# Kernel tuning notes

Measured on AMD Instinct MI355X. Metric: run time of the kernel, lower is better.

## Reference

```python
import jax, jax.numpy as jnp
import numpy as np
from jax import lax

T, B = 256, 64
VOCAB, EMB, HID, NLAB = 100000, 300, 256, 20
PAD_WORD = 0


def setup_inputs() -> dict:
    key = jax.random.key(0)
    ks = jax.random.split(key, 16)
    sentences = jax.random.randint(ks[0], (T, B), 0, VOCAB)
    sentences = sentences.at[0].set(jnp.maximum(sentences[0], 1))  # mask[0] must be all on (torchcrf)
    labels = jax.random.randint(ks[1], (T, B), 0, NLAB)
    s = 0.05
    emb = jax.random.normal(ks[2], (VOCAB, EMB), jnp.float32) * s
    Wih_f = jax.random.normal(ks[3], (4 * HID, EMB), jnp.float32) * s
    Whh_f = jax.random.normal(ks[4], (4 * HID, HID), jnp.float32) * s
    b_f = jax.random.normal(ks[5], (4 * HID,), jnp.float32) * s
    Wih_b = jax.random.normal(ks[6], (4 * HID, EMB), jnp.float32) * s
    Whh_b = jax.random.normal(ks[7], (4 * HID, HID), jnp.float32) * s
    b_b = jax.random.normal(ks[8], (4 * HID,), jnp.float32) * s
    W_top = jax.random.normal(ks[9], (NLAB, 2 * HID), jnp.float32) * s
    b_top = jax.random.normal(ks[10], (NLAB,), jnp.float32) * s
    start_t = jax.random.normal(ks[11], (NLAB,), jnp.float32) * 0.1
    end_t = jax.random.normal(ks[12], (NLAB,), jnp.float32) * 0.1
    trans = jax.random.normal(ks[13], (NLAB, NLAB), jnp.float32) * 0.1
    return dict(emb=emb, Wih_f=Wih_f, Whh_f=Whh_f, b_f=b_f, Wih_b=Wih_b,
                Whh_b=Whh_b, b_b=b_b, W_top=W_top, b_top=b_top,
                start_t=start_t, end_t=end_t, trans=trans,
                sentences=sentences, labels=labels)


def _lstm_dir(x, W_ih, W_hh, b, reverse):
    # x: (T, B, E) -> hs: (T, B, H); torch gate order i,f,g,o
    H = W_hh.shape[1]
    x_proj = jnp.einsum('tbe,ge->tbg', x, W_ih) + b  # precompute input projection

    def step(carry, xp):
        h, c = carry
        gates = xp + h @ W_hh.T
        i, f, g, o = jnp.split(gates, 4, axis=-1)
        c = jax.nn.sigmoid(f) * c + jax.nn.sigmoid(i) * jnp.tanh(g)
        h = jax.nn.sigmoid(o) * jnp.tanh(c)
        return (h, c), h

    init = (jnp.zeros((x.shape[1], H), x.dtype), jnp.zeros((x.shape[1], H), x.dtype))
    _, hs = lax.scan(step, init, x_proj, reverse=reverse)
    return hs


def _crf_nll(emissions, tags, mask, start_t, end_t, trans):
    # emissions: (T,B,L), tags: (T,B), mask: (T,B) bool. torchcrf math, reduction='sum'.
    Tn, Bn, L = emissions.shape
    maskf = mask.astype(emissions.dtype)
    barange = jnp.arange(Bn)
    # numerator
    score = start_t[tags[0]] + emissions[0, barange, tags[0]]
    trans_sc = trans[tags[:-1], tags[1:]]  # (T-1, B)
    emit_sc = jnp.take_along_axis(emissions[1:], tags[1:, :, None], axis=2)[..., 0]
    score = score + ((trans_sc + emit_sc) * maskf[1:]).sum(0)
    seq_ends = mask.astype(jnp.int32).sum(0) - 1  # (B,)
    last_tags = jnp.take_along_axis(tags, seq_ends[None, :], axis=0)[0]
    score = score + end_t[last_tags]
    # partition (log-sum-exp forward recurrence)
    alpha0 = start_t[None, :] + emissions[0]  # (B, L)

    def step(alpha, inp):
        emis_t, m_t = inp
        nxt = jax.nn.logsumexp(alpha[:, :, None] + trans[None] + emis_t[:, None, :], axis=1)
        return jnp.where(m_t[:, None], nxt, alpha), None

    alpha, _ = lax.scan(step, alpha0, (emissions[1:], mask[1:]))
    denom = jax.nn.logsumexp(alpha + end_t[None, :], axis=1)
    llh = (score - denom).sum()
    return -llh


def reference(emb, Wih_f, Whh_f, b_f, Wih_b, Whh_b, b_b, W_top, b_top,
              start_t, end_t, trans, sentences, labels):
    x = emb[sentences]  # (T, B, E)
    h_f = _lstm_dir(x, Wih_f, Whh_f, b_f, reverse=False)
    h_b = _lstm_dir(x, Wih_b, Whh_b, b_b, reverse=True)
    rnn_out = jnp.concatenate([h_f, h_b], axis=-1)  # (T, B, 2H)
    emissions = jnp.einsum('tbh,lh->tbl', rnn_out, W_top) + b_top
    mask = sentences != PAD_WORD
    return _crf_nll(emissions, labels, mask, start_t, end_t, trans)
```

## Files before the change

### kernel.cpp

```cpp
#include <hip/hip_runtime.h>
#include <hip/hip_bf16.h>

#define T_    256
#define B_    64
#define EMB_  300
#define HID_  256
#define G_    1024
#define L_    20
#define M_    (T_*B_)

#define NCL   32
#define CLB   8
#define BPC   4
#define UPB   32

typedef float f32x4 __attribute__((ext_vector_type(4)));
typedef unsigned long long u64;

__global__ __launch_bounds__(256) void k_xproj(
    const float* __restrict__ emb,
    const float* __restrict__ Wih_f, const float* __restrict__ b_f,
    const float* __restrict__ Wih_b, const float* __restrict__ b_b,
    const int*   __restrict__ sent,
    float* __restrict__ xp)
{
    __shared__ float As[16][68];
    __shared__ float Bs[16][68];
    __shared__ int   words[64];

    const int tid = threadIdx.x;
    const int n0  = blockIdx.x * 64;
    const int m0  = blockIdx.y * 64;
    const int dir = n0 >> 10;
    const int g0  = n0 & 1023;
    const float* __restrict__ Wih  = dir ? Wih_b : Wih_f;
    const float* __restrict__ bias = dir ? b_b   : b_f;

    if (tid < 64) words[tid] = sent[m0 + tid];
    __syncthreads();

    const int r = tid >> 2;
    const int q = tid & 3;
    const float* aptr = emb + (size_t)words[r] * EMB_ + q * 4;
    const float* bptr = Wih + (size_t)(g0 + r) * EMB_ + q * 4;

    const int tx = tid & 15;
    const int ty = tid >> 4;
    float acc[4][4] = {};

    for (int k0 = 0; k0 < 304; k0 += 16) {
        const int k = k0 + q * 4;
        float4 av = make_float4(0.f, 0.f, 0.f, 0.f);
        float4 bv = make_float4(0.f, 0.f, 0.f, 0.f);
        if (k < 300) {
            av = *(const float4*)(aptr + k0);
            bv = *(const float4*)(bptr + k0);
        }
        As[q*4+0][r] = av.x; As[q*4+1][r] = av.y; As[q*4+2][r] = av.z; As[q*4+3][r] = av.w;
        Bs[q*4+0][r] = bv.x; Bs[q*4+1][r] = bv.y; Bs[q*4+2][r] = bv.z; Bs[q*4+3][r] = bv.w;
        __syncthreads();
        #pragma unroll
        for (int kk = 0; kk < 16; ++kk) {
            const float4 a = *(const float4*)&As[kk][ty * 4];
            const float4 b = *(const float4*)&Bs[kk][tx * 4];
            acc[0][0] += a.x*b.x; acc[0][1] += a.x*b.y; acc[0][2] += a.x*b.z; acc[0][3] += a.x*b.w;
            acc[1][0] += a.y*b.x; acc[1][1] += a.y*b.y; acc[1][2] += a.y*b.z; acc[1][3] += a.y*b.w;
            acc[2][0] += a.z*b.x; acc[2][1] += a.z*b.y; acc[2][2] += a.z*b.z; acc[2][3] += a.z*b.w;
            acc[3][0] += a.w*b.x; acc[3][1] += a.w*b.y; acc[3][2] += a.w*b.z; acc[3][3] += a.w*b.w;
        }
        __syncthreads();
    }

    float* out = xp + (size_t)dir * M_ * G_;
    const int g = g0 + tx * 4;
    const float4 bs4 = *(const float4*)(bias + g);
    #pragma unroll
    for (int im = 0; im < 4; ++im) {
        const int m = m0 + ty * 4 + im;
        float4 rv;
        rv.x = acc[im][0] + bs4.x;
        rv.y = acc[im][1] + bs4.y;
        rv.z = acc[im][2] + bs4.z;
        rv.w = acc[im][3] + bs4.w;
        *(float4*)(out + (size_t)m * G_ + g) = rv;
    }
}

__global__ __launch_bounds__(256, 1) void k_lstm_scan(
    const float* __restrict__ Whh_f, const float* __restrict__ Whh_b,
    const float* __restrict__ xp, float* __restrict__ hbuf,
    u64* __restrict__ xch)
{
    const int rank = blockIdx.x & 7;
    const int cl   = blockIdx.x >> 3;
    const int dir  = cl >> 4;
    const int bg   = cl & 15;
    const int b0   = bg * BPC;
    const int u0   = rank * UPB;
    const int tid  = threadIdx.x;
    const int lane = tid & 63;
    const int w    = tid >> 6;
    const int kh   = lane & 1;
    const int gb0  = (lane >> 1) & 1;
    const int gb1  = (lane >> 2) & 1;
    const int g    = (lane >> 1) & 3;
    const int u_loc = (w << 3) | (lane >> 3);

    const float* __restrict__ Whh = dir ? Whh_b : Whh_f;
    const float* __restrict__ xpd = xp + (size_t)dir * M_ * G_;
    float* __restrict__ hdir = hbuf + (size_t)dir * M_ * HID_;
    u64* __restrict__ xc = xch + ((size_t)dir * B_ + b0) * HID_;

    __shared__ float hs[2][BPC][264];

    for (int i = tid; i < BPC * 264; i += 256) ((float*)hs[0])[i] = 0.f;

    f32x4 wv[32];
    {
        const f32x4* wrow = (const f32x4*)(Whh + (size_t)(g * HID_ + u0 + u_loc) * HID_ + kh * 128);
        #pragma unroll
        for (int i = 0; i < 32; ++i) wv[i] = wrow[i];
    }
    __syncthreads();

    float c_reg = 0.f;
    const int act = (kh == 0);

    for (int t = 0; t < T_; ++t) {
        const int t_eff = dir ? (T_ - 1 - t) : t;

        #pragma unroll
        for (int i = 0; i < 32; ++i) asm volatile("" : "+v"(wv[i]));

        float x0 = 0.f, x1 = 0.f, x2 = 0.f, x3 = 0.f;
        if (act) {
            const float* xrow = xpd + ((size_t)t_eff * B_ + (b0 + g)) * G_ + (u0 + u_loc);
            x0 = xrow[0]; x1 = xrow[HID_]; x2 = xrow[2 * HID_]; x3 = xrow[3 * HID_];
        }

        if (t > 0) {
            const unsigned want = (unsigned)t;
            u64 v[4];
            #pragma unroll
            for (int i = 0; i < 4; ++i)
                v[i] = __hip_atomic_load(&xc[(size_t)i * HID_ + tid],
                                         __ATOMIC_RELAXED, __HIP_MEMORY_SCOPE_AGENT);
            while ((unsigned)(v[0] >> 32) != want || (unsigned)(v[1] >> 32) != want ||
                   (unsigned)(v[2] >> 32) != want || (unsigned)(v[3] >> 32) != want) {
                #pragma unroll
                for (int i = 0; i < 4; ++i)
                    if ((unsigned)(v[i] >> 32) != want)
                        v[i] = __hip_atomic_load(&xc[(size_t)i * HID_ + tid],
                                                 __ATOMIC_RELAXED, __HIP_MEMORY_SCOPE_AGENT);
            }
            float* hw = (float*)hs[t & 1];
            #pragma unroll
            for (int i = 0; i < 4; ++i)
                hw[i * 264 + ((tid >> 7) * 132) + (tid & 127)] =
                    __uint_as_float((unsigned)v[i]);
        }
        __syncthreads();

        float a[4];
        #pragma unroll
        for (int b = 0; b < BPC; ++b) {
            const f32x4* hv = (const f32x4*)((const float*)hs[t & 1] + b * 264 + kh * 132);
            float acc = 0.f;
            #pragma unroll
            for (int i = 0; i < 32; ++i) {
                const f32x4 w4 = wv[i];
                const f32x4 h4 = hv[i];
                acc += w4.x * h4.x + w4.y * h4.y + w4.z * h4.z + w4.w * h4.w;
            }
            acc += __shfl_xor(acc, 1);
            a[b] = acc;
        }

        const float s01 = gb0 ? a[0] : a[1];
        const float r01 = __shfl_xor(s01, 2);
        const float n0 = gb0 ? r01 : a[0];
        const float n1 = gb0 ? a[1] : r01;
        const float s23 = gb0 ? a[2] : a[3];
        const float r23 = __shfl_xor(s23, 2);
        const float n2 = gb0 ? r23 : a[2];
        const float n3 = gb0 ? a[3] : r23;
        const float s02 = gb1 ? n0 : n2;
        const float r02 = __shfl_xor(s02, 4);
        const float p0 = gb1 ? r02 : n0;
        const float p2 = gb1 ? n2 : r02;
        const float s13 = gb1 ? n1 : n3;
        const float r13 = __shfl_xor(s13, 4);
        const float p1 = gb1 ? r13 : n1;
        const float p3 = gb1 ? n3 : r13;

        if (act) {
            const float gi = p0 + x0;
            const float gf = p1 + x1;
            const float gg = p2 + x2;
            const float go = p3 + x3;
            const float i_ = 1.f / (1.f + __expf(-gi));
            const float f_ = 1.f / (1.f + __expf(-gf));
            const float g_ = tanhf(gg);
            const float o_ = 1.f / (1.f + __expf(-go));
            const float cn = f_ * c_reg + i_ * g_;
            const float hn = o_ * tanhf(cn);
            c_reg = cn;
            if (t + 1 < T_) {
                const u64 pkv = ((u64)(unsigned)(t + 1) << 32) | __float_as_uint(hn);
                __hip_atomic_store(&xc[(size_t)g * HID_ + (u0 + u_loc)], pkv,
                                   __ATOMIC_RELAXED, __HIP_MEMORY_SCOPE_AGENT);
            }
            hdir[((size_t)t_eff * B_ + (b0 + g)) * HID_ + (u0 + u_loc)] = hn;
        }
    }
}

__global__ __launch_bounds__(256) void k_emis(
    const float* __restrict__ Wt, const float* __restrict__ bt,
    const float* __restrict__ hbuf, float* __restrict__ em)
{
    const int gid = blockIdx.x * 256 + threadIdx.x;
    if (gid >= M_ * L_) return;
    const int m = gid / L_;
    const int l = gid - m * L_;
    const float4* hf  = (const float4*)(hbuf + (size_t)m * HID_);
    const float4* hbk = (const float4*)(hbuf + (size_t)M_ * HID_ + (size_t)m * HID_);
    const float4* w0  = (const float4*)(Wt + (size_t)l * 2 * HID_);
    const float4* w1  = w0 + HID_ / 4;
    float acc = bt[l];
    #pragma unroll 4
    for (int k = 0; k < HID_ / 4; ++k) {
        float4 h = hf[k],  w = w0[k];
        acc += h.x*w.x + h.y*w.y + h.z*w.z + h.w*w.w;
        h = hbk[k]; w = w1[k];
        acc += h.x*w.x + h.y*w.y + h.z*w.z + h.w*w.w;
    }
    em[gid] = acc;
}

__global__ __launch_bounds__(64) void k_crf(
    const float* __restrict__ start_t, const float* __restrict__ end_t,
    const float* __restrict__ trans,
    const int* __restrict__ sent, const int* __restrict__ labels,
    const float* __restrict__ em, float* __restrict__ res)
{
    const int b = blockIdx.x;
    const int tid = threadIdx.x;
    __shared__ float tr[L_ * L_];
    __shared__ float alpha[2][L_];
    __shared__ float red[64];
    __shared__ int   redi[64];
    __shared__ float sdenom;

    for (int i = tid; i < L_ * L_; i += 64) tr[i] = trans[i];
    if (tid < L_) alpha[0][tid] = start_t[tid] + em[b * L_ + tid];
    __syncthreads();

    float pre_em = (tid < L_) ? em[(B_ + b) * L_ + tid] : 0.f;
    int   pre_m  = sent[B_ + b];

    int p = 0;
    for (int t = 1; t < T_; ++t) {
        const float emt = pre_em;
        const int   mt  = pre_m;
        if (t + 1 < T_) {
            if (tid < L_) pre_em = em[((t + 1) * B_ + b) * L_ + tid];
            pre_m = sent[(t + 1) * B_ + b];
        }
        float val = 0.f;
        if (tid < L_) {
            if (mt != 0) {
                float mx = -1e30f;
                #pragma unroll
                for (int i = 0; i < L_; ++i) mx = fmaxf(mx, alpha[p][i] + tr[i * L_ + tid]);
                float s = 0.f;
                #pragma unroll
                for (int i = 0; i < L_; ++i) s += __expf(alpha[p][i] + tr[i * L_ + tid] - mx);
                val = mx + __logf(s) + emt;
            } else {
                val = alpha[p][tid];
            }
        }
        if (tid < L_) alpha[1 - p][tid] = val;
        __syncthreads();
        p ^= 1;
    }

    if (tid == 0) {
        float mx = -1e30f;
        for (int j = 0; j < L_; ++j) mx = fmaxf(mx, alpha[p][j] + end_t[j]);
        float s = 0.f;
        for (int j = 0; j < L_; ++j) s += __expf(alpha[p][j] + end_t[j] - mx);
        sdenom = mx + __logf(s);
    }

    float loc = 0.f;
    int   cnt = 0;
    for (int t = tid; t < T_; t += 64) {
        const int masked = (sent[t * B_ + b] != 0);
        cnt += masked;
        if (t >= 1 && masked) {
            const int tp = labels[(t - 1) * B_ + b];
            const int tc = labels[t * B_ + b];
            loc += tr[tp * L_ + tc] + em[(t * B_ + b) * L_ + tc];
        }
    }
    red[tid] = loc; redi[tid] = cnt;
    __syncthreads();
    if (tid == 0) {
        float s = 0.f; int c = 0;
        for (int i = 0; i < 64; ++i) { s += red[i]; c += redi[i]; }
        const int tag0 = labels[b];
        const int seq_end = c - 1;
        const int last = labels[seq_end * B_ + b];
        const float score = start_t[tag0] + em[b * L_ + tag0] + s + end_t[last];
        res[b] = score - sdenom;
    }
}

__global__ __launch_bounds__(64) void k_final(const float* __restrict__ res,
                                              float* __restrict__ out)
{
    __shared__ float red[64];
    red[threadIdx.x] = res[threadIdx.x];
    __syncthreads();
    if (threadIdx.x == 0) {
        float s = 0.f;
        for (int i = 0; i < 64; ++i) s += red[i];
        out[0] = -s;
    }
}

extern "C" void kernel_launch(void* const* d_in, const int* in_sizes, int n_in,
                              void* d_out, int out_size, void* d_ws, size_t ws_size,
                              hipStream_t stream)
{
    const float* emb     = (const float*)d_in[0];
    const float* Wih_f   = (const float*)d_in[1];
    const float* Whh_f   = (const float*)d_in[2];
    const float* b_f     = (const float*)d_in[3];
    const float* Wih_b   = (const float*)d_in[4];
    const float* Whh_b   = (const float*)d_in[5];
    const float* b_b     = (const float*)d_in[6];
    const float* W_top   = (const float*)d_in[7];
    const float* b_top   = (const float*)d_in[8];
    const float* start_t = (const float*)d_in[9];
    const float* end_t   = (const float*)d_in[10];
    const float* trans   = (const float*)d_in[11];
    const int*   sent    = (const int*)d_in[12];
    const int*   labels  = (const int*)d_in[13];
    float* out = (float*)d_out;

    float* wsf  = (float*)d_ws;
    float* xp   = wsf;
    float* hbuf = xp   + (size_t)2 * M_ * G_;
    float* em   = hbuf + (size_t)2 * M_ * HID_;
    float* res  = em   + (size_t)M_ * L_;
    u64*   xch  = (u64*)(res + 64);

    k_xproj<<<dim3(2048 / 64, M_ / 64), 256, 0, stream>>>(
        emb, Wih_f, b_f, Wih_b, b_b, sent, xp);

    {
        void* args[] = { (void*)&Whh_f, (void*)&Whh_b, (void*)&xp, (void*)&hbuf, (void*)&xch };
        hipLaunchCooperativeKernel((const void*)k_lstm_scan, dim3(256), dim3(256),
                                   args, 0, stream);
    }

    k_emis<<<(M_ * L_ + 255) / 256, 256, 0, stream>>>(W_top, b_top, hbuf, em);

    k_crf<<<B_, 64, 0, stream>>>(start_t, end_t, trans, sent, labels, em, res);

    k_final<<<1, 64, 0, stream>>>(res, out);
}
```

Measured before the change: 1.799 ms.

## Pipeline per-batch-row hidden exchange with double-buffered slots in LSTM scan

The recurrent LSTM scan now waits for, computes and publishes each of its four batch rows separately instead of waiting on all four exchanged hidden vectors before any matvec. Exchange buffers are double-buffered by step parity so the next step's values can be prefetched, and the gate transpose shuffles are restructured per batch row. This aims to overlap cross-block communication latency with compute along the serial dependency chain, at the cost of four block barriers per step instead of one and changes to exchange buffer indexing.

```diff
diff --git a/kernel.cpp b/kernel.cpp
--- a/kernel.cpp
+++ b/kernel.cpp
@@ -101,15 +101,13 @@
     const int lane = tid & 63;
     const int w    = tid >> 6;
     const int kh   = lane & 1;
-    const int gb0  = (lane >> 1) & 1;
-    const int gb1  = (lane >> 2) & 1;
     const int g    = (lane >> 1) & 3;
     const int u_loc = (w << 3) | (lane >> 3);
 
     const float* __restrict__ Whh = dir ? Whh_b : Whh_f;
     const float* __restrict__ xpd = xp + (size_t)dir * M_ * G_;
     float* __restrict__ hdir = hbuf + (size_t)dir * M_ * HID_;
-    u64* __restrict__ xc = xch + ((size_t)dir * B_ + b0) * HID_;
+    u64* __restrict__ xc = xch + (size_t)cl * 2048;
 
     __shared__ float hs[2][BPC][264];
 
@@ -124,7 +122,7 @@
     __syncthreads();
 
     float c_reg = 0.f;
-    const int act = (kh == 0);
+    u64 vv[4] = {0ull, 0ull, 0ull, 0ull};
 
     for (int t = 0; t < T_; ++t) {
         const int t_eff = dir ? (T_ - 1 - t) : t;
@@ -133,38 +131,36 @@
         for (int i = 0; i < 32; ++i) asm volatile("" : "+v"(wv[i]));
 
         float x0 = 0.f, x1 = 0.f, x2 = 0.f, x3 = 0.f;
-        if (act) {
+        if (kh == 0) {
             const float* xrow = xpd + ((size_t)t_eff * B_ + (b0 + g)) * G_ + (u0 + u_loc);
             x0 = xrow[0]; x1 = xrow[HID_]; x2 = xrow[2 * HID_]; x3 = xrow[3 * HID_];
         }
 
-        if (t > 0) {
-            const unsigned want = (unsigned)t;
-            u64 v[4];
-            #pragma unroll
-            for (int i = 0; i < 4; ++i)
-                v[i] = __hip_atomic_load(&xc[(size_t)i * HID_ + tid],
-                                         __ATOMIC_RELAXED, __HIP_MEMORY_SCOPE_AGENT);
-            while ((unsigned)(v[0] >> 32) != want || (unsigned)(v[1] >> 32) != want ||
-                   (unsigned)(v[2] >> 32) != want || (unsigned)(v[3] >> 32) != want) {
-                #pragma unroll
-                for (int i = 0; i < 4; ++i)
-                    if ((unsigned)(v[i] >> 32) != want)
-                        v[i] = __hip_atomic_load(&xc[(size_t)i * HID_ + tid],
-                                                 __ATOMIC_RELAXED, __HIP_MEMORY_SCOPE_AGENT);
-            }
-            float* hw = (float*)hs[t & 1];
-            #pragma unroll
-            for (int i = 0; i < 4; ++i)
-                hw[i * 264 + ((tid >> 7) * 132) + (tid & 127)] =
-                    __uint_as_float((unsigned)v[i]);
-        }
-        __syncthreads();
-
-        float a[4];
+        u64* const slot_cur = xc + (size_t)(t & 1) * 1024;
+        u64* const slot_nxt = xc + (size_t)((t + 1) & 1) * 1024;
+        float* const hcur = (float*)hs[t & 1];
+
         #pragma unroll
-        for (int b = 0; b < BPC; ++b) {
-            const f32x4* hv = (const f32x4*)((const float*)hs[t & 1] + b * 264 + kh * 132);
+        for (int b = 0; b < 4; ++b) {
+            {
+                const int wn = (b + 2) & 3;
+                u64* const sp = (b >= 2) ? slot_nxt : slot_cur;
+                vv[wn] = __hip_atomic_load(&sp[(size_t)wn * 256 + tid],
+                                           __ATOMIC_RELAXED, __HIP_MEMORY_SCOPE_AGENT);
+            }
+
+            if (t > 0) {
+                const unsigned want = (unsigned)t;
+                u64 v = vv[b];
+                while ((unsigned)(v >> 32) != want)
+                    v = __hip_atomic_load(&slot_cur[(size_t)b * 256 + tid],
+                                          __ATOMIC_RELAXED, __HIP_MEMORY_SCOPE_AGENT);
+                hcur[b * 264 + (tid >> 7) * 132 + (tid & 127)] =
+                    __uint_as_float((unsigned)v);
+            }
+            __syncthreads();
+
+            const f32x4* hv = (const f32x4*)(hcur + b * 264 + kh * 132);
             float acc = 0.f;
             #pragma unroll
             for (int i = 0; i < 32; ++i) {
@@ -173,44 +169,31 @@
                 acc += w4.x * h4.x + w4.y * h4.y + w4.z * h4.z + w4.w * h4.w;
             }
             acc += __shfl_xor(acc, 1);
-            a[b] = acc;
-        }
-
-        const float s01 = gb0 ? a[0] : a[1];
-        const float r01 = __shfl_xor(s01, 2);
-        const float n0 = gb0 ? r01 : a[0];
-        const float n1 = gb0 ? a[1] : r01;
-        const float s23 = gb0 ? a[2] : a[3];
-        const float r23 = __shfl_xor(s23, 2);
-        const float n2 = gb0 ? r23 : a[2];
-        const float n3 = gb0 ? a[3] : r23;
-        const float s02 = gb1 ? n0 : n2;
-        const float r02 = __shfl_xor(s02, 4);
-        const float p0 = gb1 ? r02 : n0;
-        const float p2 = gb1 ? n2 : r02;
-        const float s13 = gb1 ? n1 : n3;
-        const float r13 = __shfl_xor(s13, 4);
-        const float p1 = gb1 ? r13 : n1;
-        const float p3 = gb1 ? n3 : r13;
-
-        if (act) {
-            const float gi = p0 + x0;
-            const float gf = p1 + x1;
-            const float gg = p2 + x2;
-            const float go = p3 + x3;
-            const float i_ = 1.f / (1.f + __expf(-gi));
-            const float f_ = 1.f / (1.f + __expf(-gf));
-            const float g_ = tanhf(gg);
-            const float o_ = 1.f / (1.f + __expf(-go));
-            const float cn = f_ * c_reg + i_ * g_;
-            const float hn = o_ * tanhf(cn);
-            c_reg = cn;
-            if (t + 1 < T_) {
-                const u64 pkv = ((u64)(unsigned)(t + 1) << 32) | __float_as_uint(hn);
-                __hip_atomic_store(&xc[(size_t)g * HID_ + (u0 + u_loc)], pkv,
-                                   __ATOMIC_RELAXED, __HIP_MEMORY_SCOPE_AGENT);
-            }
-            hdir[((size_t)t_eff * B_ + (b0 + g)) * HID_ + (u0 + u_loc)] = hn;
+
+            const float v1 = __shfl_xor(acc, 2);
+            const float v2 = __shfl_xor(acc, 4);
+            const float v3 = __shfl_xor(v1, 4);
+
+            if (g == b && kh == 0) {
+                const float arr[4] = {acc, v1, v2, v3};
+                const float gi = arr[b ^ 0] + x0;
+                const float gf = arr[b ^ 1] + x1;
+                const float gg = arr[b ^ 2] + x2;
+                const float go = arr[b ^ 3] + x3;
+                const float i_ = 1.f / (1.f + __expf(-gi));
+                const float f_ = 1.f / (1.f + __expf(-gf));
+                const float g_ = tanhf(gg);
+                const float o_ = 1.f / (1.f + __expf(-go));
+                const float cn = f_ * c_reg + i_ * g_;
+                const float hn = o_ * tanhf(cn);
+                c_reg = cn;
+                if (t + 1 < T_) {
+                    const u64 pkv = ((u64)(unsigned)(t + 1) << 32) | __float_as_uint(hn);
+                    __hip_atomic_store(&slot_nxt[(size_t)b * 256 + (u0 + u_loc)], pkv,
+                                       __ATOMIC_RELAXED, __HIP_MEMORY_SCOPE_AGENT);
+                }
+                hdir[((size_t)t_eff * B_ + (b0 + b)) * HID_ + (u0 + u_loc)] = hn;
+            }
         }
     }
 }
```

Measured after the change: 2.093 ms. +16.3%, slower.

## Add XCD-local fast exchange path with sc0 polling and atomic fallback

Applied to the files above, without the earlier changes.

Block-to-cluster mapping changes so the 8 ranks of a cluster are spaced 32 block IDs apart, likely placing them on the same XCD under round-robin dispatch. Each step's hidden state is written twice, once as a plain store to a fast buffer and once as an agent-scope atomic to a backup buffer, both double-buffered by timestep parity. Readers poll the fast buffer with sc0 loads, which may be served from a cache shared by the cluster, for up to a bounded number of spins. If that bound is exceeded they switch permanently to the agent-scope atomic path. The aim is lower inter-block exchange latency in the serial LSTM recurrence, at the cost of extra stores and reliance on the dispatch placement and cache coherence behaviour.

```diff
diff --git a/kernel.cpp b/kernel.cpp
--- a/kernel.cpp
+++ b/kernel.cpp
@@ -13,9 +13,25 @@
 #define CLB   8
 #define BPC   4
 #define UPB   32
+#define SPIN_MAX 768
 
 typedef float f32x4 __attribute__((ext_vector_type(4)));
 typedef unsigned long long u64;
+
+__device__ __forceinline__ void ld4_sc0(const u64* p0, const u64* p1,
+                                        const u64* p2, const u64* p3,
+                                        u64& a, u64& b, u64& c, u64& d)
+{
+    asm volatile(
+        "global_load_dwordx2 %0, %4, off sc0\n\t"
+        "global_load_dwordx2 %1, %5, off sc0\n\t"
+        "global_load_dwordx2 %2, %6, off sc0\n\t"
+        "global_load_dwordx2 %3, %7, off sc0\n\t"
+        "s_waitcnt vmcnt(0)"
+        : "=&v"(a), "=&v"(b), "=&v"(c), "=&v"(d)
+        : "v"(p0), "v"(p1), "v"(p2), "v"(p3)
+        : "memory");
+}
 
 __global__ __launch_bounds__(256) void k_xproj(
     const float* __restrict__ emb,
@@ -91,8 +107,8 @@
     const float* __restrict__ xp, float* __restrict__ hbuf,
     u64* __restrict__ xch)
 {
-    const int rank = blockIdx.x & 7;
-    const int cl   = blockIdx.x >> 3;
+    const int cl   = blockIdx.x & 31;
+    const int rank = blockIdx.x >> 5;
     const int dir  = cl >> 4;
     const int bg   = cl & 15;
     const int b0   = bg * BPC;
@@ -109,11 +125,12 @@
     const float* __restrict__ Whh = dir ? Whh_b : Whh_f;
     const float* __restrict__ xpd = xp + (size_t)dir * M_ * G_;
     float* __restrict__ hdir = hbuf + (size_t)dir * M_ * HID_;
-    u64* __restrict__ xc = xch + ((size_t)dir * B_ + b0) * HID_;
+    u64* __restrict__ xcF = xch + (size_t)cl * 2048;
+    u64* __restrict__ xcB = xch + (size_t)NCL * 2048 + (size_t)cl * 2048;
 
     __shared__ float hs[2][BPC][264];
 
-    for (int i = tid; i < BPC * 264; i += 256) ((float*)hs[0])[i] = 0.f;
+    for (int i = tid; i < BPC * 264; i += 256) ((float*)hs)[i] = 0.f;
 
     f32x4 wv[32];
     {
@@ -125,6 +142,7 @@
 
     float c_reg = 0.f;
     const int act = (kh == 0);
+    int fastmode = 1;
 
     for (int t = 0; t < T_; ++t) {
         const int t_eff = dir ? (T_ - 1 - t) : t;
@@ -140,24 +158,44 @@
 
         if (t > 0) {
             const unsigned want = (unsigned)t;
-            u64 v[4];
-            #pragma unroll
-            for (int i = 0; i < 4; ++i)
-                v[i] = __hip_atomic_load(&xc[(size_t)i * HID_ + tid],
-                                         __ATOMIC_RELAXED, __HIP_MEMORY_SCOPE_AGENT);
-            while ((unsigned)(v[0] >> 32) != want || (unsigned)(v[1] >> 32) != want ||
-                   (unsigned)(v[2] >> 32) != want || (unsigned)(v[3] >> 32) != want) {
+            u64 v0 = 0, v1 = 0, v2 = 0, v3 = 0;
+            bool got = false;
+
+            if (fastmode) {
+                const u64* sl = xcF + (size_t)(t & 1) * 1024;
+                for (int s = 0; s < SPIN_MAX; ++s) {
+                    ld4_sc0(sl + tid, sl + 256 + tid, sl + 512 + tid, sl + 768 + tid,
+                            v0, v1, v2, v3);
+                    if ((unsigned)(v0 >> 32) == want && (unsigned)(v1 >> 32) == want &&
+                        (unsigned)(v2 >> 32) == want && (unsigned)(v3 >> 32) == want) {
+                        got = true; break;
+                    }
+                }
+                if (!got) fastmode = 0;
+            }
+            if (!got) {
+                const u64* bl = xcB + (size_t)(t & 1) * 1024;
+                u64 vb[4];
                 #pragma unroll
                 for (int i = 0; i < 4; ++i)
-                    if ((unsigned)(v[i] >> 32) != want)
-                        v[i] = __hip_atomic_load(&xc[(size_t)i * HID_ + tid],
-                                                 __ATOMIC_RELAXED, __HIP_MEMORY_SCOPE_AGENT);
+                    vb[i] = __hip_atomic_load(&bl[(size_t)i * 256 + tid],
+                                              __ATOMIC_RELAXED, __HIP_MEMORY_SCOPE_AGENT);
+                while ((unsigned)(vb[0] >> 32) != want || (unsigned)(vb[1] >> 32) != want ||
+                       (unsigned)(vb[2] >> 32) != want || (unsigned)(vb[3] >> 32) != want) {
+                    #pragma unroll
+                    for (int i = 0; i < 4; ++i)
+                        if ((unsigned)(vb[i] >> 32) != want)
+                            vb[i] = __hip_atomic_load(&bl[(size_t)i * 256 + tid],
+                                                      __ATOMIC_RELAXED, __HIP_MEMORY_SCOPE_AGENT);
+                }
+                v0 = vb[0]; v1 = vb[1]; v2 = vb[2]; v3 = vb[3];
             }
+
             float* hw = (float*)hs[t & 1];
-            #pragma unroll
-            for (int i = 0; i < 4; ++i)
-                hw[i * 264 + ((tid >> 7) * 132) + (tid & 127)] =
-                    __uint_as_float((unsigned)v[i]);
+            hw[0 * 264 + ((tid >> 7) * 132) + (tid & 127)] = __uint_as_float((unsigned)v0);
+            hw[1 * 264 + ((tid >> 7) * 132) + (tid & 127)] = __uint_as_float((unsigned)v1);
+            hw[2 * 264 + ((tid >> 7) * 132) + (tid & 127)] = __uint_as_float((unsigned)v2);
+            hw[3 * 264 + ((tid >> 7) * 132) + (tid & 127)] = __uint_as_float((unsigned)v3);
         }
         __syncthreads();
 
@@ -207,7 +245,9 @@
             c_reg = cn;
             if (t + 1 < T_) {
                 const u64 pkv = ((u64)(unsigned)(t + 1) << 32) | __float_as_uint(hn);
-                __hip_atomic_store(&xc[(size_t)g * HID_ + (u0 + u_loc)], pkv,
+                const size_t widx = (size_t)((t + 1) & 1) * 1024 + (size_t)g * 256 + (u0 + u_loc);
+                xcF[widx] = pkv;
+                __hip_atomic_store(&xcB[widx], pkv,
                                    __ATOMIC_RELAXED, __HIP_MEMORY_SCOPE_AGENT);
             }
             hdir[((size_t)t_eff * B_ + (b0 + g)) * HID_ + (u0 + u_loc)] = hn;
```

New measurement: 3.125 ms. 73.7% more time.

## Double-buffer LSTM hidden-state exchange slots and stage emission inputs in shared memory

Applied to the files above, without the earlier changes.

The cross-block hidden-state exchange in the cooperative LSTM scan now alternates between two slot buffers by timestep parity, with a per-cluster region of 2048 entries. This lets a fast producer write step t+1 without overwriting values a slower consumer still needs for step t, which removes a write-after-read hazard and its spin stalls. The emission kernel now loads 16 rows of forward and backward hidden state into padded shared memory per block and computes all 20 labels from there with 320 threads, so each hidden row is read from global memory once instead of twenty times. The exchange buffer needs twice the workspace, and the emission kernel now uses more shared memory per block.

```diff
diff --git a/kernel.cpp b/kernel.cpp
--- a/kernel.cpp
+++ b/kernel.cpp
@@ -109,11 +109,11 @@
     const float* __restrict__ Whh = dir ? Whh_b : Whh_f;
     const float* __restrict__ xpd = xp + (size_t)dir * M_ * G_;
     float* __restrict__ hdir = hbuf + (size_t)dir * M_ * HID_;
-    u64* __restrict__ xc = xch + ((size_t)dir * B_ + b0) * HID_;
+    u64* __restrict__ xc = xch + (size_t)cl * 2048;
 
     __shared__ float hs[2][BPC][264];
 
-    for (int i = tid; i < BPC * 264; i += 256) ((float*)hs[0])[i] = 0.f;
+    for (int i = tid; i < BPC * 264; i += 256) ((float*)hs)[i] = 0.f;
 
     f32x4 wv[32];
     {
@@ -140,17 +140,18 @@
 
         if (t > 0) {
             const unsigned want = (unsigned)t;
+            const u64* sl = xc + (size_t)(t & 1) * 1024;
             u64 v[4];
             #pragma unroll
             for (int i = 0; i < 4; ++i)
-                v[i] = __hip_atomic_load(&xc[(size_t)i * HID_ + tid],
+                v[i] = __hip_atomic_load(&sl[(size_t)i * 256 + tid],
                                          __ATOMIC_RELAXED, __HIP_MEMORY_SCOPE_AGENT);
             while ((unsigned)(v[0] >> 32) != want || (unsigned)(v[1] >> 32) != want ||
                    (unsigned)(v[2] >> 32) != want || (unsigned)(v[3] >> 32) != want) {
                 #pragma unroll
                 for (int i = 0; i < 4; ++i)
                     if ((unsigned)(v[i] >> 32) != want)
-                        v[i] = __hip_atomic_load(&xc[(size_t)i * HID_ + tid],
+                        v[i] = __hip_atomic_load(&sl[(size_t)i * 256 + tid],
                                                  __ATOMIC_RELAXED, __HIP_MEMORY_SCOPE_AGENT);
             }
             float* hw = (float*)hs[t & 1];
@@ -207,35 +208,46 @@
             c_reg = cn;
             if (t + 1 < T_) {
                 const u64 pkv = ((u64)(unsigned)(t + 1) << 32) | __float_as_uint(hn);
-                __hip_atomic_store(&xc[(size_t)g * HID_ + (u0 + u_loc)], pkv,
-                                   __ATOMIC_RELAXED, __HIP_MEMORY_SCOPE_AGENT);
+                __hip_atomic_store(&xc[(size_t)((t + 1) & 1) * 1024 + (size_t)g * 256 + (u0 + u_loc)],
+                                   pkv, __ATOMIC_RELAXED, __HIP_MEMORY_SCOPE_AGENT);
             }
             hdir[((size_t)t_eff * B_ + (b0 + g)) * HID_ + (u0 + u_loc)] = hn;
         }
     }
 }
 
-__global__ __launch_bounds__(256) void k_emis(
+__global__ __launch_bounds__(320) void k_emis(
     const float* __restrict__ Wt, const float* __restrict__ bt,
     const float* __restrict__ hbuf, float* __restrict__ em)
 {
-    const int gid = blockIdx.x * 256 + threadIdx.x;
-    if (gid >= M_ * L_) return;
-    const int m = gid / L_;
-    const int l = gid - m * L_;
-    const float4* hf  = (const float4*)(hbuf + (size_t)m * HID_);
-    const float4* hbk = (const float4*)(hbuf + (size_t)M_ * HID_ + (size_t)m * HID_);
-    const float4* w0  = (const float4*)(Wt + (size_t)l * 2 * HID_);
-    const float4* w1  = w0 + HID_ / 4;
+    __shared__ float4 hfS[16][65];
+    __shared__ float4 hbS[16][65];
+
+    const int tid = threadIdx.x;
+    const int m0  = blockIdx.x * 16;
+
+    for (int idx = tid; idx < 16 * 64; idx += 320) {
+        const int mm = idx >> 6;
+        const int kk = idx & 63;
+        hfS[mm][kk] = ((const float4*)(hbuf + (size_t)(m0 + mm) * HID_))[kk];
+        hbS[mm][kk] = ((const float4*)(hbuf + (size_t)M_ * HID_ + (size_t)(m0 + mm) * HID_))[kk];
+    }
+    __syncthreads();
+
+    const int m = tid / L_;
+    const int l = tid - m * L_;
+
+    const float4* w0 = (const float4*)(Wt + (size_t)l * 2 * HID_);
+    const float4* w1 = w0 + HID_ / 4;
     float acc = bt[l];
     #pragma unroll 4
     for (int k = 0; k < HID_ / 4; ++k) {
-        float4 h = hf[k],  w = w0[k];
+        float4 h = hfS[m][k], w = w0[k];
         acc += h.x*w.x + h.y*w.y + h.z*w.z + h.w*w.w;
-        h = hbk[k]; w = w1[k];
+        h = hbS[m][k]; w = w1[k];
         acc += h.x*w.x + h.y*w.y + h.z*w.z + h.w*w.w;
     }
-    em[gid] = acc;
+    em[(size_t)(m0 + m) * L_ + l] = acc;
 }
 
 __global__ __launch_bounds__(64) void k_crf(
@@ -367,7 +379,7 @@
                                    args, 0, stream);
     }
 
-    k_emis<<<(M_ * L_ + 255) / 256, 256, 0, stream>>>(W_top, b_top, hbuf, em);
+    k_emis<<<M_ / 16, 320, 0, stream>>>(W_top, b_top, hbuf, em);
 
     k_crf<<<B_, 64, 0, stream>>>(start_t, end_t, trans, sent, labels, em, res);
 
```

Result: slower. 1.867 ms (+3.8%).
